# Kernel optimization log

Hardware: AMD Instinct MI355X
Metric: run time of the kernel (lower is better)

The kernel has to match this reference:

```python
import jax, jax.numpy as jnp
import numpy as np

STATE_DIM = 64   # state_dim (N), N/2 complex modes
KLEN = 128       # L, learned impulse-response length
CH = 1           # channel_dim
BATCH = 32
T = 1048576      # sequence length (T > L -> FFT branch)
DT_MIN, DT_MAX = 0.001, 0.1


def setup_inputs() -> dict:
    key = jax.random.key(0)
    ks = jax.random.split(key, 7)
    N2 = STATE_DIM // 2
    x = jax.random.normal(ks[0], (BATCH, CH, T), dtype=jnp.float32)
    # HiPPO initialization: w = -0.5 + i * (1/pi) * N * (N/(1+2k) - 1)
    k = np.arange(N2)
    w_real = np.broadcast_to(np.float32(-0.5), (CH, N2)).copy()
    w_imag = np.broadcast_to(
        ((1.0 / np.pi) * STATE_DIM * (STATE_DIM / (1.0 + 2.0 * k) - 1.0)).astype(np.float32),
        (CH, N2)).copy()
    log_dt = (jax.random.uniform(ks[1], (CH, 1), dtype=jnp.float32)
              * (np.log(DT_MAX) - np.log(DT_MIN)) + np.log(DT_MIN))
    C_real = jax.random.normal(ks[2], (CH, 1, N2), dtype=jnp.float32) * 0.1
    C_imag = jax.random.normal(ks[3], (CH, 1, N2), dtype=jnp.float32) * 0.1
    B_real = jax.random.normal(ks[4], (CH, N2), dtype=jnp.float32)
    B_imag = jax.random.normal(ks[5], (CH, N2), dtype=jnp.float32)
    nrm = jnp.sqrt(jnp.sum(B_real ** 2 + B_imag ** 2, axis=-1, keepdims=True))
    B_real, B_imag = B_real / nrm, B_imag / nrm
    D = jax.random.normal(ks[6], (CH,), dtype=jnp.float32) * 0.1
    return {"azimuth_data": x,
            "w_real": jnp.asarray(w_real), "w_imag": jnp.asarray(w_imag),
            "log_dt": log_dt,
            "C_real": C_real, "C_imag": C_imag,
            "B_real": B_real, "B_imag": B_imag,
            "D": D}


def _ssm_kernel(w_real, w_imag, log_dt, C_real, C_imag, B_real, B_imag, D, L):
    """Vectorized equivalent of the per-step power recurrence: h_k = Re(sum_n C_n B_n A_n^k)."""
    w = w_real + 1j * w_imag                      # (CH, N2) complex eigenvalues
    dt = jnp.exp(log_dt)                          # (CH, 1)
    Cc = C_real + 1j * C_imag                     # (CH, 1, N2)
    Bc = B_real + 1j * B_imag                     # (CH, N2)
    dtA = dt[..., None] * w                       # (CH,1,1)*(CH,N2) -> (CH,1,N2)
    # coefficients C.squeeze(1) * B, with the same broadcast as torch: (CH,N2)*(CH,1,N2)->(CH,1,N2)
    coef = jnp.squeeze(Cc, axis=1) * (jnp.ones_like(dtA) * Bc)   # (CH,1,N2)
    ks = jnp.arange(L, dtype=dtA.real.dtype)                      # (L,)
    Ak = jnp.exp(dtA[..., None] * ks)                             # (CH,1,N2,L) = A_discrete**k
    h = jnp.real(jnp.sum(coef[..., None] * Ak, axis=-2))          # (CH,1,L)
    h = h.at[..., 0].add(D)                                       # hk[0] += D (broadcast (CH,1)+(CH,))
    return h[:, None]                                             # unsqueeze(1) -> (CH,1,1,L)


def reference(azimuth_data, w_real, w_imag, log_dt, C_real, C_imag, B_real, B_imag, D):
    Bsz, Cn, Tn = azimuth_data.shape
    kernel = _ssm_kernel(w_real, w_imag, log_dt, C_real, C_imag, B_real, B_imag, D, KLEN)
    pad = KLEN - 1
    x_padded = jnp.pad(azimuth_data, ((0, 0), (0, 0), (pad, 0)))   # causal left-pad
    L_conv = x_padded.shape[-1]
    x_f = jnp.fft.rfft(x_padded, n=L_conv)                         # (B, CH, F)
    k_f = jnp.fft.rfft(kernel, n=L_conv)                           # (CH, 1, 1, F)
    y_f = x_f * k_f                                                # broadcast -> (CH, B, 1, F)
    focused = jnp.fft.irfft(y_f, n=L_conv)[..., :Tn]               # (CH, B, 1, T) — matches torch broadcast
    return focused
```

## Files before the change

kernel.cpp:

```cpp
#include <hip/hip_runtime.h>

#define T_LEN  1048576
#define NROWS  32
#define NTAPS  128
#define N2     32
#define BLOCK  256
#define SEG    4096
#define SPB    8
#define HALO   256
#define NCH    11
#define STG_CH 1088

typedef __attribute__((ext_vector_type(8)))  _Float16 half8;
typedef __attribute__((ext_vector_type(2)))  __fp16   fp16x2;
typedef __attribute__((ext_vector_type(16))) float    f32x16;

__device__ __forceinline__ int swz(int q) { return q ^ ((q >> 3) & 7); }

__device__ __forceinline__ void gload_lds16(const float* g, float* l) {
  __builtin_amdgcn_global_load_lds(
      (const __attribute__((address_space(1))) void*)g,
      (__attribute__((address_space(3))) void*)l, 16, 0, 0);
}

__global__ __launch_bounds__(NTAPS) void ssm_taps(
    const float* __restrict__ w_real, const float* __restrict__ w_imag,
    const float* __restrict__ log_dt,
    const float* __restrict__ C_real, const float* __restrict__ C_imag,
    const float* __restrict__ B_real, const float* __restrict__ B_imag,
    const float* __restrict__ Dp, float* __restrict__ ws) {
  __shared__ float hsh[NTAPS];
  const int k = threadIdx.x;
  const float dt = expf(log_dt[0]);
  const float kf = (float)k;
  float acc = 0.f;
  for (int n = 0; n < N2; ++n) {
    const float a  = dt * w_real[n];
    const float b  = dt * w_imag[n];
    const float cr = C_real[n], ci = C_imag[n];
    const float br = B_real[n], bi = B_imag[n];
    const float coef_r = cr * br - ci * bi;
    const float coef_i = cr * bi + ci * br;
    const float e = expf(a * kf);
    float s, c;
    sincosf(b * kf, &s, &c);
    acc += e * (coef_r * c - coef_i * s);
  }
  if (k == 0) acc += Dp[0];
  ws[k]  = acc;
  hsh[k] = acc;
  __syncthreads();
  if (k < 64) {
    _Float16* AH = (_Float16*)(ws + NTAPS);
    const int m = k & 31, g = k >> 5;
    for (int c = 0; c < NCH; ++c)
      for (int i = 0; i < 8; ++i) {
        const int idx = m + 129 - 16 * c - 8 * g - i;
        const float v = (idx >= 0 && idx < NTAPS) ? hsh[idx] : 0.f;
        AH[(c * 64 + k) * 8 + i] = (_Float16)v;
      }
  }
}

__global__ __launch_bounds__(BLOCK, 4) void ssm_conv(
    const float* __restrict__ x, const float* __restrict__ ws,
    float* __restrict__ out) {
  __shared__ __align__(16) float lds[2][STG_CH * 4];

  const int tid  = threadIdx.x;
  const int lane = tid & 63;
  const int wid  = tid >> 6;
  const int p    = lane & 31, g = lane >> 5;
  const int row  = blockIdx.x >> 5;
  const int jb   = blockIdx.x & 31;
  const float* __restrict__ xrow = x + (size_t)row * T_LEN;

  half8 A[NCH];
  const half8* __restrict__ wsA = (const half8*)(ws + NTAPS);
#pragma unroll
  for (int c = 0; c < NCH; ++c) A[c] = wsA[c * 64 + lane];

  int n0 = jb * (SPB * SEG);

  auto stage = [&](int b, int sn0) {
#pragma unroll
    for (int j = 0; j < 5; ++j) {
      const int ch = j * 256 + wid * 64 + lane;
      if (ch < STG_CH) {
        const int sq = swz(ch);
        int gfi = sn0 - HALO + 4 * sq;
        gfi = gfi < 0 ? 0 : gfi;
        gload_lds16(xrow + gfi, &lds[b][(j * 256 + wid * 64) * 4]);
      }
    }
  };

  stage(0, n0);
  asm volatile("s_waitcnt vmcnt(0)" ::: "memory");
  __syncthreads();

  for (int s = 0; s < SPB; ++s) {
    if (s + 1 < SPB) stage((s + 1) & 1, n0 + SEG);

    const float* __restrict__ Bb = lds[s & 1];
    f32x16 acc = {};
#pragma unroll
    for (int c = 0; c < NCH; ++c) {
      const int q0 = wid * 256 + 8 * p + 2 * g + 4 * c;
      const float4 f0 = *(const float4*)(Bb + (swz(q0) << 2));
      const float4 f1 = *(const float4*)(Bb + (swz(q0 + 1) << 2));
      union { half8 h8; unsigned u[4]; } bu;
      bu.u[0] = __builtin_bit_cast(unsigned, __builtin_amdgcn_cvt_pkrtz(f0.x, f0.y));
      bu.u[1] = __builtin_bit_cast(unsigned, __builtin_amdgcn_cvt_pkrtz(f0.z, f0.w));
      bu.u[2] = __builtin_bit_cast(unsigned, __builtin_amdgcn_cvt_pkrtz(f1.x, f1.y));
      bu.u[3] = __builtin_bit_cast(unsigned, __builtin_amdgcn_cvt_pkrtz(f1.z, f1.w));
      acc = __builtin_amdgcn_mfma_f32_32x32x16_f16(A[c], bu.h8, acc, 0, 0, 0);
    }

    float* __restrict__ orow =
        out + (size_t)row * T_LEN + n0 + wid * 1024 + 32 * p + 4 * g;
#pragma unroll
    for (int kq = 0; kq < 4; ++kq) {
      float4 v;
      v.x = acc[4 * kq];     v.y = acc[4 * kq + 1];
      v.z = acc[4 * kq + 2]; v.w = acc[4 * kq + 3];
      *(float4*)(orow + 8 * kq) = v;
    }

    if (s + 1 < SPB) {
      asm volatile("s_waitcnt vmcnt(4)" ::: "memory");
      __syncthreads();
    }
    n0 += SEG;
  }
}

__global__ __launch_bounds__(BLOCK) void ssm_fix(
    const float* __restrict__ x, const float* __restrict__ ws,
    float* __restrict__ out) {
  const int row = blockIdx.x;
  const int n = threadIdx.x;
  const float* __restrict__ h = ws;
  const float* __restrict__ xrow = x + (size_t)row * T_LEN;
  float acc = 0.f;
  if (n < 127) {
    for (int k = n + 1; k < NTAPS; ++k)
      acc += h[k] * xrow[T_LEN + n - k];
  } else if (n < 254) {
    for (int k = 0; k <= n - 127; ++k)
      acc += h[k] * xrow[n - 127 - k];
  } else {
    return;
  }
  out[(size_t)row * T_LEN + n] = acc;
}

extern "C" void kernel_launch(void* const* d_in, const int* in_sizes, int n_in,
                              void* d_out, int out_size, void* d_ws, size_t ws_size,
                              hipStream_t stream) {
  const float* x      = (const float*)d_in[0];
  const float* w_real = (const float*)d_in[1];
  const float* w_imag = (const float*)d_in[2];
  const float* log_dt = (const float*)d_in[3];
  const float* C_real = (const float*)d_in[4];
  const float* C_imag = (const float*)d_in[5];
  const float* B_real = (const float*)d_in[6];
  const float* B_imag = (const float*)d_in[7];
  const float* Dp     = (const float*)d_in[8];
  float* out = (float*)d_out;
  float* ws  = (float*)d_ws;

  ssm_taps<<<1, NTAPS, 0, stream>>>(w_real, w_imag, log_dt,
                                    C_real, C_imag, B_real, B_imag, Dp, ws);
  ssm_conv<<<NROWS * 32, BLOCK, 0, stream>>>(x, ws, out);
  ssm_fix<<<NROWS, BLOCK, 0, stream>>>(x, ws, out);
}
```

Baseline: 72.25 us.

## Launch one block per segment instead of persistent double-buffered loop

Replaces the per-block loop over eight segments with software double buffering by a grid of one block per 4096-sample segment, using a single LDS buffer and higher occupancy (launch bounds 8). This relies on hardware block-level parallelism for latency hiding instead of explicit prefetch. In exchange, each block reloads the A fragments and the 256-sample halo, and pays per-block launch and drain overhead.

```diff
diff --git a/kernel.cpp b/kernel.cpp
--- a/kernel.cpp
+++ b/kernel.cpp
@@ -6,7 +6,7 @@
 #define N2     32
 #define BLOCK  256
 #define SEG    4096
-#define SPB    8
+#define SEGS_PER_ROW 256
 #define HALO   256
 #define NCH    11
 #define STG_CH 1088
@@ -62,76 +62,56 @@
   }
 }
 
-__global__ __launch_bounds__(BLOCK, 4) void ssm_conv(
+__global__ __launch_bounds__(BLOCK, 8) void ssm_conv(
     const float* __restrict__ x, const float* __restrict__ ws,
     float* __restrict__ out) {
-  __shared__ __align__(16) float lds[2][STG_CH * 4];
+  __shared__ __align__(16) float lds[STG_CH * 4];
 
   const int tid  = threadIdx.x;
   const int lane = tid & 63;
   const int wid  = tid >> 6;
   const int p    = lane & 31, g = lane >> 5;
-  const int row  = blockIdx.x >> 5;
-  const int jb   = blockIdx.x & 31;
+  const int row  = blockIdx.x >> 8;
+  const int jb   = blockIdx.x & 255;
+  const int n0   = jb * SEG;
   const float* __restrict__ xrow = x + (size_t)row * T_LEN;
+  const half8* __restrict__ wsA = (const half8*)(ws + NTAPS);
 
-  half8 A[NCH];
-  const half8* __restrict__ wsA = (const half8*)(ws + NTAPS);
 #pragma unroll
-  for (int c = 0; c < NCH; ++c) A[c] = wsA[c * 64 + lane];
-
-  int n0 = jb * (SPB * SEG);
-
-  auto stage = [&](int b, int sn0) {
-#pragma unroll
-    for (int j = 0; j < 5; ++j) {
-      const int ch = j * 256 + wid * 64 + lane;
-      if (ch < STG_CH) {
-        const int sq = swz(ch);
-        int gfi = sn0 - HALO + 4 * sq;
-        gfi = gfi < 0 ? 0 : gfi;
-        gload_lds16(xrow + gfi, &lds[b][(j * 256 + wid * 64) * 4]);
-      }
+  for (int j = 0; j < 5; ++j) {
+    const int ch = j * 256 + wid * 64 + lane;
+    if (ch < STG_CH) {
+      int gfi = n0 - HALO + 4 * swz(ch);
+      gfi = gfi < 0 ? 0 : gfi;
+      gload_lds16(xrow + gfi, &lds[(j * 256 + wid * 64) * 4]);
     }
-  };
-
-  stage(0, n0);
+  }
   asm volatile("s_waitcnt vmcnt(0)" ::: "memory");
   __syncthreads();
 
-  for (int s = 0; s < SPB; ++s) {
-    if (s + 1 < SPB) stage((s + 1) & 1, n0 + SEG);
+  f32x16 acc = {};
+#pragma unroll
+  for (int c = 0; c < NCH; ++c) {
+    const half8 A = wsA[c * 64 + lane];
+    const int q0 = wid * 256 + 8 * p + 2 * g + 4 * c;
+    const float4 f0 = *(const float4*)(lds + (swz(q0) << 2));
+    const float4 f1 = *(const float4*)(lds + (swz(q0 + 1) << 2));
+    union { half8 h8; unsigned u[4]; } bu;
+    bu.u[0] = __builtin_bit_cast(unsigned, __builtin_amdgcn_cvt_pkrtz(f0.x, f0.y));
+    bu.u[1] = __builtin_bit_cast(unsigned, __builtin_amdgcn_cvt_pkrtz(f0.z, f0.w));
+    bu.u[2] = __builtin_bit_cast(unsigned, __builtin_amdgcn_cvt_pkrtz(f1.x, f1.y));
+    bu.u[3] = __builtin_bit_cast(unsigned, __builtin_amdgcn_cvt_pkrtz(f1.z, f1.w));
+    acc = __builtin_amdgcn_mfma_f32_32x32x16_f16(A, bu.h8, acc, 0, 0, 0);
+  }
 
-    const float* __restrict__ Bb = lds[s & 1];
-    f32x16 acc = {};
+  float* __restrict__ orow =
+      out + (size_t)row * T_LEN + n0 + wid * 1024 + 32 * p + 4 * g;
 #pragma unroll
-    for (int c = 0; c < NCH; ++c) {
-      const int q0 = wid * 256 + 8 * p + 2 * g + 4 * c;
-      const float4 f0 = *(const float4*)(Bb + (swz(q0) << 2));
-      const float4 f1 = *(const float4*)(Bb + (swz(q0 + 1) << 2));
-      union { half8 h8; unsigned u[4]; } bu;
-      bu.u[0] = __builtin_bit_cast(unsigned, __builtin_amdgcn_cvt_pkrtz(f0.x, f0.y));
-      bu.u[1] = __builtin_bit_cast(unsigned, __builtin_amdgcn_cvt_pkrtz(f0.z, f0.w));
-      bu.u[2] = __builtin_bit_cast(unsigned, __builtin_amdgcn_cvt_pkrtz(f1.x, f1.y));
-      bu.u[3] = __builtin_bit_cast(unsigned, __builtin_amdgcn_cvt_pkrtz(f1.z, f1.w));
-      acc = __builtin_amdgcn_mfma_f32_32x32x16_f16(A[c], bu.h8, acc, 0, 0, 0);
-    }
-
-    float* __restrict__ orow =
-        out + (size_t)row * T_LEN + n0 + wid * 1024 + 32 * p + 4 * g;
-#pragma unroll
-    for (int kq = 0; kq < 4; ++kq) {
-      float4 v;
-      v.x = acc[4 * kq];     v.y = acc[4 * kq + 1];
-      v.z = acc[4 * kq + 2]; v.w = acc[4 * kq + 3];
-      *(float4*)(orow + 8 * kq) = v;
-    }
-
-    if (s + 1 < SPB) {
-      asm volatile("s_waitcnt vmcnt(4)" ::: "memory");
-      __syncthreads();
-    }
-    n0 += SEG;
+  for (int kq = 0; kq < 4; ++kq) {
+    float4 v;
+    v.x = acc[4 * kq];     v.y = acc[4 * kq + 1];
+    v.z = acc[4 * kq + 2]; v.w = acc[4 * kq + 3];
+    *(float4*)(orow + 8 * kq) = v;
   }
 }
 
@@ -172,6 +152,6 @@
 
   ssm_taps<<<1, NTAPS, 0, stream>>>(w_real, w_imag, log_dt,
                                     C_real, C_imag, B_real, B_imag, Dp, ws);
-  ssm_conv<<<NROWS * 32, BLOCK, 0, stream>>>(x, ws, out);
+  ssm_conv<<<NROWS * SEGS_PER_ROW, BLOCK, 0, stream>>>(x, ws, out);
   ssm_fix<<<NROWS, BLOCK, 0, stream>>>(x, ws, out);
 }
```

Result: slower. 74.36 us (+2.9%).
